# Kernel optimization log

Measured on AMD Instinct MI355X. Metric: run time of the kernel, lower is better.

The kernel has to match this reference:

```python
import jax, jax.numpy as jnp
import numpy as np

B, S, H, NH, L, V, P = 2, 1024, 768, 12, 4, 32000, 1024
HD = H // NH  # head dim = 64; matches scale_val = hidden/num_heads


def setup_inputs() -> dict:
    key = jax.random.key(0)
    ks = jax.random.split(key, 18)
    sc = 0.02
    n = jax.random.normal
    return {
        "input_ids": jax.random.randint(ks[0], (B, S), 0, V, dtype=jnp.int32),
        "seq_mask": jnp.ones((B, S), jnp.float32),
        "bpe_emb": (n(ks[1], (V, H)) * sc).astype(jnp.float32),
        "pos_emb": (n(ks[2], (P, H)) * sc).astype(jnp.float32),
        "qkv_w": (n(ks[3], (L, H, 3 * H)) * sc).astype(jnp.float32),
        "qkv_b": jnp.zeros((L, 3 * H), jnp.float32),
        "res_w": (n(ks[4], (L, H, H)) * sc).astype(jnp.float32),
        "res_b": jnp.zeros((L, H), jnp.float32),
        "ln1_g": jnp.ones((L, H), jnp.float32),
        "ln1_b": jnp.zeros((L, H), jnp.float32),
        "ff1_w": (n(ks[5], (L, H, 4 * H)) * sc).astype(jnp.float32),
        "ff1_b": jnp.zeros((L, 4 * H), jnp.float32),
        "ff2_w": (n(ks[6], (L, 4 * H, H)) * sc).astype(jnp.float32),
        "ff2_b": jnp.zeros((L, H), jnp.float32),
        "ln2_g": jnp.ones((L, H), jnp.float32),
        "ln2_b": jnp.zeros((L, H), jnp.float32),
        "pred_w": (n(ks[7], (H, V)) * sc).astype(jnp.float32),
    }


def _layer_norm(x, g, b, e=1e-5):
    u = jnp.mean(x, -1, keepdims=True)
    s = jnp.mean((x - u) ** 2, -1, keepdims=True)
    return g * ((x - u) / jnp.sqrt(s + e)) + b


def _attention(x, seq_mask, w_qkv, b_qkv, w_res, b_res):
    qkv = x @ w_qkv + b_qkv                    # [B,S,3H]
    q, k, v = jnp.split(qkv, 3, axis=-1)
    q = q.reshape(B, S, NH, HD)
    k = k.reshape(B, S, NH, HD)
    v = v.reshape(B, S, NH, HD)
    score = jnp.einsum('bqhd,bkhd->bhqk', q, k) / jnp.sqrt(jnp.float32(HD))
    tril = jnp.tril(jnp.ones((S, S), jnp.float32))           # causal
    mask = tril[None, None] * seq_mask[:, None, None, :]      # [B,1,S,S]
    score = score + (1.0 - mask) * -1e9
    prob = jax.nn.softmax(score, axis=-1)      # dropout rate 0 -> identity
    val = jnp.einsum('bhqk,bkhd->bqhd', prob, v).reshape(B, S, H)
    return val @ w_res + b_res                 # dropout rate 0 -> identity


def reference(input_ids, seq_mask, bpe_emb, pos_emb, qkv_w, qkv_b, res_w, res_b,
              ln1_g, ln1_b, ff1_w, ff1_b, ff2_w, ff2_b, ln2_g, ln2_b, pred_w):
    pos_idx = jnp.arange(S)
    h = bpe_emb[input_ids] + pos_emb[pos_idx][None]           # [B,S,H]
    for l in range(L):
        a = _attention(h, seq_mask, qkv_w[l], qkv_b[l], res_w[l], res_b[l])
        h = _layer_norm(h + a, ln1_g[l], ln1_b[l])
        m = (jax.nn.gelu(h @ ff1_w[l] + ff1_b[l], approximate=False)
             @ ff2_w[l] + ff2_b[l])
        h = _layer_norm(h + m, ln2_g[l], ln2_b[l])
    pred_score = h @ pred_w                                   # [B,S,V]
    pred_prob = jax.nn.softmax(pred_score, axis=-1)
    return pred_score, pred_prob
```

## Files before the change

kernel.cpp:

```cpp
#include <hip/hip_runtime.h>
#include <math.h>

#define BB 2
#define SS 1024
#define HH 768
#define NHEAD 12
#define HDIM 64
#define NLAYER 4
#define VV 32000
#define MROWS (BB*SS)

typedef unsigned short u16;
typedef __attribute__((ext_vector_type(8))) short short8;
typedef __attribute__((ext_vector_type(4))) float f32x4;
typedef __attribute__((ext_vector_type(4))) unsigned short u16x4;

__device__ __forceinline__ u16 f2bf(float f) {
    union { float f; unsigned u; } x; x.f = f;
    unsigned r = (x.u + 0x7fff + ((x.u >> 16) & 1)) >> 16;
    return (u16)r;
}
__device__ __forceinline__ float bf2f(u16 b) {
    union { unsigned u; float f; } x; x.u = ((unsigned)b) << 16;
    return x.f;
}

__device__ __forceinline__ void gload_lds16(const u16* g, u16* l) {
    __builtin_amdgcn_global_load_lds((const __attribute__((address_space(1))) void*)g,
                                     (__attribute__((address_space(3))) void*)l, 16, 0, 0);
}

__global__ __launch_bounds__(256) void conv_transpose(
    const float* __restrict__ W, u16* __restrict__ Wt, int K, int N) {
    int l = blockIdx.z;
    W  += (size_t)l * K * N;
    Wt += (size_t)l * K * N;
    __shared__ u16 tile[32][33];
    int k0 = blockIdx.y * 32, n0 = blockIdx.x * 32;
    int t = threadIdx.x;
    int ky = t >> 3, nx = (t & 7) * 4;
    float4 v = *(const float4*)(W + (size_t)(k0 + ky) * N + n0 + nx);
    tile[nx + 0][ky] = f2bf(v.x);
    tile[nx + 1][ky] = f2bf(v.y);
    tile[nx + 2][ky] = f2bf(v.z);
    tile[nx + 3][ky] = f2bf(v.w);
    __syncthreads();
    int nr = t >> 3, kc = (t & 7) * 4;
    u16x4 o;
    o[0] = tile[nr][kc + 0]; o[1] = tile[nr][kc + 1];
    o[2] = tile[nr][kc + 2]; o[3] = tile[nr][kc + 3];
    *(u16x4*)(Wt + (size_t)(n0 + nr) * K + k0 + kc) = o;
}

__global__ void embed_kernel(const int* __restrict__ ids,
                             const float* __restrict__ bpe,
                             const float* __restrict__ pos,
                             float* __restrict__ h, u16* __restrict__ hb) {
    int row = blockIdx.x;
    int s = row % SS;
    int id = ids[row];
    const float4* br = (const float4*)(bpe + (size_t)id * HH);
    const float4* pr = (const float4*)(pos + (size_t)s * HH);
    float4* hr = (float4*)(h + (size_t)row * HH);
    u16x4* hbr = (u16x4*)(hb + (size_t)row * HH);
    int t = threadIdx.x;
    float4 a = br[t], c = pr[t];
    a.x += c.x; a.y += c.y; a.z += c.z; a.w += c.w;
    hr[t] = a;
    u16x4 u; u[0] = f2bf(a.x); u[1] = f2bf(a.y); u[2] = f2bf(a.z); u[3] = f2bf(a.w);
    hbr[t] = u;
}

template<int BM, int ACT, int WF32, int WBF>
__global__ __launch_bounds__(256) void mfma_gemm(
    const u16* __restrict__ A, const u16* __restrict__ Wt,
    const float* __restrict__ bias, float* __restrict__ C,
    u16* __restrict__ Cb, int M, int N, int K) {
    constexpr int MR = BM / 32;
    __shared__ u16 As[2 * BM * 32];
    __shared__ u16 Bs[2 * 128 * 32];
    const int tid = threadIdx.x;
    const int lane = tid & 63;
    const int wid = tid >> 6;

    const int nwg = gridDim.x * gridDim.y;
    int id = blockIdx.x + gridDim.x * blockIdx.y;
    int id2 = (nwg & 7) ? id : ((id & 7) * (nwg >> 3) + (id >> 3));
    const int brow = (id2 % gridDim.x) * BM;
    const int bcol = (id2 / gridDim.x) * 128;

    const int wr = (wid >> 1) * (BM / 2);
    const int wc = (wid & 1) * 64;
    f32x4 acc[MR][4] = {};

    const u16* Abase = A + (size_t)brow * K;
    const u16* Bbase = Wt + (size_t)bcol * K;
    const int lrow = lane & 15;
    const int lk = (lane >> 4) * 8;

    auto stage = [&](u16* Ad, u16* Bd, int kt) {
#pragma unroll
        for (int c0 = 0; c0 < BM * 4; c0 += 256) {
            int c = c0 + tid;
            int r = c >> 2, off = (c & 3) * 8;
            gload_lds16(Abase + (size_t)r * K + kt + off, Ad + c * 8);
        }
#pragma unroll
        for (int c0 = 0; c0 < 512; c0 += 256) {
            int c = c0 + tid;
            int r = c >> 2, off = (c & 3) * 8;
            gload_lds16(Bbase + (size_t)r * K + kt + off, Bd + c * 8);
        }
    };

    const int nt = K / 32;
    stage(As, Bs, 0);
    for (int t = 0; t < nt; ++t) {
        u16* Ac = As + (t & 1) * (BM * 32);
        u16* Bc = Bs + (t & 1) * (128 * 32);
        if (t + 1 < nt) {
            stage(As + ((t + 1) & 1) * (BM * 32),
                  Bs + ((t + 1) & 1) * (128 * 32), (t + 1) * 32);
            if constexpr (BM == 128) asm volatile("s_waitcnt vmcnt(4)" ::: "memory");
            else                     asm volatile("s_waitcnt vmcnt(3)" ::: "memory");
        } else {
            asm volatile("s_waitcnt vmcnt(0)" ::: "memory");
        }
        __builtin_amdgcn_s_barrier();
        __builtin_amdgcn_sched_barrier(0);

        short8 a[MR], b[4];
#pragma unroll
        for (int m = 0; m < MR; ++m)
            a[m] = *(const short8*)(Ac + (wr + m * 16 + lrow) * 32 + lk);
#pragma unroll
        for (int n = 0; n < 4; ++n)
            b[n] = *(const short8*)(Bc + (wc + n * 16 + lrow) * 32 + lk);
#pragma unroll
        for (int m = 0; m < MR; ++m)
#pragma unroll
            for (int n = 0; n < 4; ++n)
                acc[m][n] = __builtin_amdgcn_mfma_f32_16x16x32_bf16(a[m], b[n], acc[m][n], 0, 0, 0);

        __builtin_amdgcn_sched_barrier(0);
        __builtin_amdgcn_s_barrier();
    }

    const int lr4 = (lane >> 4) * 4;
#pragma unroll
    for (int n = 0; n < 4; ++n) {
        int col = bcol + wc + n * 16 + lrow;
        float bv = bias ? bias[col] : 0.f;
#pragma unroll
        for (int m = 0; m < MR; ++m) {
#pragma unroll
            for (int j = 0; j < 4; ++j) {
                int row = brow + wr + m * 16 + lr4 + j;
                float v = acc[m][n][j] + bv;
                if (ACT == 1) v = 0.5f * v * (1.f + erff(v * 0.70710678118654752f));
                if (WF32) C[(size_t)row * N + col] = v;
                if (WBF)  Cb[(size_t)row * N + col] = f2bf(v);
            }
        }
    }
}

__global__ __launch_bounds__(256) void attn_kernel(
    const u16* __restrict__ qkvb, const float* __restrict__ seq_mask,
    u16* __restrict__ av) {
    __shared__ u16 Ks[64 * 64];
    __shared__ u16 Vt[64 * 64];
    __shared__ u16 Ps[64 * 64];
    const int qb = gridDim.x - 1 - blockIdx.x;
    const int hd = blockIdx.y, b = blockIdx.z;
    const int t = threadIdx.x;
    const int lane = t & 63;
    const int w = t >> 6;
    const int lrow = lane & 15;
    const int lhi = lane >> 4;
    const int q0 = qb * 64;
    const size_t rs = 3 * HH;

    short8 aq[2];
    {
        const u16* qrow = qkvb + (size_t)(b * SS + q0 + w * 16 + lrow) * rs + hd * HDIM;
        aq[0] = *(const short8*)(qrow + lhi * 8);
        aq[1] = *(const short8*)(qrow + 32 + lhi * 8);
    }

    f32x4 o[4] = {};
    float m_[4] = {-INFINITY, -INFINITY, -INFINITY, -INFINITY};
    float l_[4] = {0.f, 0.f, 0.f, 0.f};

    const int kr = t >> 2, dc = t & 3;
    short8 kA, kB, vA, vB;
    {
        const u16* kbase = qkvb + (size_t)(b * SS + kr) * rs + HH + hd * HDIM + dc * 16;
        kA = *(const short8*)(kbase);
        kB = *(const short8*)(kbase + 8);
        vA = *(const short8*)(kbase + HH);
        vB = *(const short8*)(kbase + HH + 8);
    }

    for (int kt = 0; kt <= qb; ++kt) {
        const int k0 = kt * 64;
        __syncthreads();
        {
            char* krowp = (char*)Ks + kr * 128;
            *(short8*)(krowp + (((dc * 32 + 0)  ^ ((kr & 7) << 4)))) = kA;
            *(short8*)(krowp + (((dc * 32 + 16) ^ ((kr & 7) << 4)))) = kB;
#pragma unroll
            for (int e = 0; e < 8; ++e) {
                int d0 = dc * 16 + e;
                int d1 = dc * 16 + 8 + e;
                *(u16*)((char*)Vt + d0 * 128 + ((kr * 2) ^ ((d0 & 7) << 4))) = (u16)vA[e];
                *(u16*)((char*)Vt + d1 * 128 + ((kr * 2) ^ ((d1 & 7) << 4))) = (u16)vB[e];
            }
        }
        __syncthreads();

        if (kt < qb) {
            const u16* kbase = qkvb + (size_t)(b * SS + k0 + 64 + kr) * rs + HH + hd * HDIM + dc * 16;
            kA = *(const short8*)(kbase);
            kB = *(const short8*)(kbase + 8);
            vA = *(const short8*)(kbase + HH);
            vB = *(const short8*)(kbase + HH + 8);
        }

        f32x4 s[4] = {};
        __builtin_amdgcn_s_setprio(1);
#pragma unroll
        for (int n = 0; n < 4; ++n) {
            const int krow = n * 16 + lrow;
            char* kp = (char*)Ks + krow * 128;
#pragma unroll
            for (int c = 0; c < 2; ++c) {
                short8 bk = *(const short8*)(kp + ((c * 64 + lhi * 16) ^ ((krow & 7) << 4)));
                s[n] = __builtin_amdgcn_mfma_f32_16x16x32_bf16(aq[c], bk, s[n], 0, 0, 0);
            }
        }
        __builtin_amdgcn_s_setprio(0);

        float sm[4];
#pragma unroll
        for (int n = 0; n < 4; ++n) sm[n] = seq_mask[b * SS + k0 + n * 16 + lrow];
        const int diag = (kt == qb);
#pragma unroll
        for (int j = 0; j < 4; ++j) {
            const int qglob = q0 + w * 16 + lhi * 4 + j;
            float sv[4];
#pragma unroll
            for (int n = 0; n < 4; ++n) {
                const int kglob = k0 + n * 16 + lrow;
                float msk = (diag && kglob > qglob) ? 0.f : sm[n];
                sv[n] = s[n][j] * 0.125f + (1.f - msk) * (-1e9f);
            }
            float tm = fmaxf(fmaxf(sv[0], sv[1]), fmaxf(sv[2], sv[3]));
            tm = fmaxf(tm, __shfl_xor(tm, 1));
            tm = fmaxf(tm, __shfl_xor(tm, 2));
            tm = fmaxf(tm, __shfl_xor(tm, 4));
            tm = fmaxf(tm, __shfl_xor(tm, 8));
            float mn = fmaxf(m_[j], tm);
            float sc = __expf(m_[j] - mn);
            float ps = 0.f;
#pragma unroll
            for (int n = 0; n < 4; ++n) {
                float p = __expf(sv[n] - mn);
                s[n][j] = p;
                ps += p;
            }
            ps += __shfl_xor(ps, 1);
            ps += __shfl_xor(ps, 2);
            ps += __shfl_xor(ps, 4);
            ps += __shfl_xor(ps, 8);
            l_[j] = l_[j] * sc + ps;
            m_[j] = mn;
#pragma unroll
            for (int dn = 0; dn < 4; ++dn) o[dn][j] *= sc;
        }

#pragma unroll
        for (int j = 0; j < 4; ++j) {
            const int prow = w * 16 + lhi * 4 + j;
            char* pp = (char*)Ps + prow * 128;
#pragma unroll
            for (int n = 0; n < 4; ++n)
                *(u16*)(pp + ((n * 32 + lrow * 2) ^ ((prow & 7) << 4))) = f2bf(s[n][j]);
        }

        const int arow = w * 16 + lrow;
        char* ap_p = (char*)Ps + arow * 128;
        __builtin_amdgcn_s_setprio(1);
#pragma unroll
        for (int c = 0; c < 2; ++c) {
            short8 ap = *(const short8*)(ap_p + ((c * 64 + lhi * 16) ^ ((arow & 7) << 4)));
#pragma unroll
            for (int dn = 0; dn < 4; ++dn) {
                const int vrow = dn * 16 + lrow;
                short8 bv = *(const short8*)((char*)Vt + vrow * 128 +
                                             ((c * 64 + lhi * 16) ^ ((vrow & 7) << 4)));
                o[dn] = __builtin_amdgcn_mfma_f32_16x16x32_bf16(ap, bv, o[dn], 0, 0, 0);
            }
        }
        __builtin_amdgcn_s_setprio(0);
    }

#pragma unroll
    for (int j = 0; j < 4; ++j) {
        const int q = q0 + w * 16 + lhi * 4 + j;
        const float inv = 1.f / l_[j];
        u16* orow = av + (size_t)(b * SS + q) * HH + hd * HDIM;
#pragma unroll
        for (int dn = 0; dn < 4; ++dn)
            orow[dn * 16 + lrow] = f2bf(o[dn][j] * inv);
    }
}

__global__ void add_ln_kernel(float* __restrict__ h, u16* __restrict__ hb,
                              const float* __restrict__ a,
                              const float* __restrict__ g,
                              const float* __restrict__ bta) {
    int row = blockIdx.x;
    int t = threadIdx.x;
    __shared__ float red[256];
    size_t base = (size_t)row * HH;
    float x0 = h[base + t]       + a[base + t];
    float x1 = h[base + t + 256] + a[base + t + 256];
    float x2 = h[base + t + 512] + a[base + t + 512];

    red[t] = x0 + x1 + x2;
    __syncthreads();
    for (int o = 128; o; o >>= 1) { if (t < o) red[t] += red[t + o]; __syncthreads(); }
    float mean = red[0] * (1.0f / 768.0f);
    __syncthreads();

    float d0 = x0 - mean, d1 = x1 - mean, d2 = x2 - mean;
    red[t] = d0 * d0 + d1 * d1 + d2 * d2;
    __syncthreads();
    for (int o = 128; o; o >>= 1) { if (t < o) red[t] += red[t + o]; __syncthreads(); }
    float var = red[0] * (1.0f / 768.0f);
    float inv = 1.0f / sqrtf(var + 1e-5f);

    float y0 = g[t]       * d0 * inv + bta[t];
    float y1 = g[t + 256] * d1 * inv + bta[t + 256];
    float y2 = g[t + 512] * d2 * inv + bta[t + 512];
    h[base + t] = y0;       hb[base + t] = f2bf(y0);
    h[base + t + 256] = y1; hb[base + t + 256] = f2bf(y1);
    h[base + t + 512] = y2; hb[base + t + 512] = f2bf(y2);
}

__global__ __launch_bounds__(512) void softmax_v_kernel(
    const float* __restrict__ score, float* __restrict__ prob) {
    __shared__ u16 srow[VV];
    __shared__ float red[512];
    int row = blockIdx.x;
    int t = threadIdx.x;
    const float4* sr = (const float4*)(score + (size_t)row * VV);
    float4* pr = (float4*)(prob + (size_t)row * VV);
    const int n4 = VV / 4;

    float mx = -INFINITY;
    for (int i = t; i < n4; i += 512) {
        float4 v = sr[i];
        u16x4 u; u[0] = f2bf(v.x); u[1] = f2bf(v.y); u[2] = f2bf(v.z); u[3] = f2bf(v.w);
        *(u16x4*)(srow + i * 4) = u;
        mx = fmaxf(mx, fmaxf(fmaxf(bf2f(u[0]), bf2f(u[1])), fmaxf(bf2f(u[2]), bf2f(u[3]))));
    }
    red[t] = mx; __syncthreads();
    for (int o = 256; o; o >>= 1) { if (t < o) red[t] = fmaxf(red[t], red[t + o]); __syncthreads(); }
    mx = red[0];
    __syncthreads();

    float s = 0.f;
    for (int i = t; i < n4; i += 512) {
        u16x4 u = *(const u16x4*)(srow + i * 4);
        s += __expf(bf2f(u[0]) - mx) + __expf(bf2f(u[1]) - mx)
           + __expf(bf2f(u[2]) - mx) + __expf(bf2f(u[3]) - mx);
    }
    red[t] = s; __syncthreads();
    for (int o = 256; o; o >>= 1) { if (t < o) red[t] += red[t + o]; __syncthreads(); }
    float inv = 1.0f / red[0];

    for (int i = t; i < n4; i += 512) {
        u16x4 u = *(const u16x4*)(srow + i * 4);
        float4 o4;
        o4.x = __expf(bf2f(u[0]) - mx) * inv; o4.y = __expf(bf2f(u[1]) - mx) * inv;
        o4.z = __expf(bf2f(u[2]) - mx) * inv; o4.w = __expf(bf2f(u[3]) - mx) * inv;
        pr[i] = o4;
    }
}

extern "C" void kernel_launch(void* const* d_in, const int* in_sizes, int n_in,
                              void* d_out, int out_size, void* d_ws, size_t ws_size,
                              hipStream_t stream) {
    const int*   ids      = (const int*)d_in[0];
    const float* seq_mask = (const float*)d_in[1];
    const float* bpe      = (const float*)d_in[2];
    const float* pos      = (const float*)d_in[3];
    const float* qkv_w    = (const float*)d_in[4];
    const float* qkv_b    = (const float*)d_in[5];
    const float* res_w    = (const float*)d_in[6];
    const float* res_b    = (const float*)d_in[7];
    const float* ln1_g    = (const float*)d_in[8];
    const float* ln1_b    = (const float*)d_in[9];
    const float* ff1_w    = (const float*)d_in[10];
    const float* ff1_b    = (const float*)d_in[11];
    const float* ff2_w    = (const float*)d_in[12];
    const float* ff2_b    = (const float*)d_in[13];
    const float* ln2_g    = (const float*)d_in[14];
    const float* ln2_b    = (const float*)d_in[15];
    const float* pred_w   = (const float*)d_in[16];

    float* out_score = (float*)d_out;
    float* out_prob  = out_score + (size_t)MROWS * VV;

    size_t off = 0;
    auto take = [&](size_t bytes) -> size_t {
        size_t p = off; off += (bytes + 255) & ~(size_t)255; return p;
    };
    const size_t o_qkvT = take((size_t)NLAYER * HH * 3 * HH * 2);
    const size_t o_resT = take((size_t)NLAYER * HH * HH * 2);
    const size_t o_ff1T = take((size_t)NLAYER * HH * 4 * HH * 2);
    const size_t o_ff2T = take((size_t)NLAYER * 4 * HH * HH * 2);
    const size_t o_predT = take((size_t)HH * VV * 2);
    const size_t o_h    = take((size_t)MROWS * HH * 4);
    const size_t o_a    = take((size_t)MROWS * HH * 4);
    const size_t o_qkvb = take((size_t)MROWS * 3 * HH * 2);
    const size_t o_hb   = take((size_t)MROWS * HH * 2);
    const size_t o_avb  = take((size_t)MROWS * HH * 2);
    const size_t o_midb = take((size_t)MROWS * 4 * HH * 2);
    const size_t need = off;

    char* arena = (ws_size >= need) ? (char*)d_ws : (char*)out_prob;
    u16*   qkvT = (u16*)(arena + o_qkvT);
    u16*   resT = (u16*)(arena + o_resT);
    u16*   ff1T = (u16*)(arena + o_ff1T);
    u16*   ff2T = (u16*)(arena + o_ff2T);
    u16*   predT = (u16*)(arena + o_predT);
    float* h    = (float*)(arena + o_h);
    float* a    = (float*)(arena + o_a);
    u16*   qkvb = (u16*)(arena + o_qkvb);
    u16*   hb   = (u16*)(arena + o_hb);
    u16*   avb  = (u16*)(arena + o_avb);
    u16*   midb = (u16*)(arena + o_midb);

    conv_transpose<<<dim3(3 * HH / 32, HH / 32, NLAYER), 256, 0, stream>>>(qkv_w, qkvT, HH, 3 * HH);
    conv_transpose<<<dim3(HH / 32, HH / 32, NLAYER), 256, 0, stream>>>(res_w, resT, HH, HH);
    conv_transpose<<<dim3(4 * HH / 32, HH / 32, NLAYER), 256, 0, stream>>>(ff1_w, ff1T, HH, 4 * HH);
    conv_transpose<<<dim3(HH / 32, 4 * HH / 32, NLAYER), 256, 0, stream>>>(ff2_w, ff2T, 4 * HH, HH);
    conv_transpose<<<dim3(VV / 32, HH / 32, 1), 256, 0, stream>>>(pred_w, predT, HH, VV);

    embed_kernel<<<MROWS, 192, 0, stream>>>(ids, bpe, pos, h, hb);

    for (int l = 0; l < NLAYER; ++l) {
        mfma_gemm<128, 0, 0, 1><<<dim3(MROWS / 128, 3 * HH / 128), 256, 0, stream>>>(
            hb, qkvT + (size_t)l * HH * 3 * HH, qkv_b + (size_t)l * 3 * HH,
            nullptr, qkvb, MROWS, 3 * HH, HH);
        attn_kernel<<<dim3(SS / 64, NHEAD, BB), 256, 0, stream>>>(qkvb, seq_mask, avb);
        mfma_gemm<64, 0, 1, 0><<<dim3(MROWS / 64, HH / 128), 256, 0, stream>>>(
            avb, resT + (size_t)l * HH * HH, res_b + (size_t)l * HH,
            a, nullptr, MROWS, HH, HH);
        add_ln_kernel<<<MROWS, 256, 0, stream>>>(h, hb, a,
            ln1_g + (size_t)l * HH, ln1_b + (size_t)l * HH);
        mfma_gemm<128, 1, 0, 1><<<dim3(MROWS / 128, 4 * HH / 128), 256, 0, stream>>>(
            hb, ff1T + (size_t)l * HH * 4 * HH, ff1_b + (size_t)l * 4 * HH,
            nullptr, midb, MROWS, 4 * HH, HH);
        mfma_gemm<64, 0, 1, 0><<<dim3(MROWS / 64, HH / 128), 256, 0, stream>>>(
            midb, ff2T + (size_t)l * 4 * HH * HH, ff2_b + (size_t)l * HH,
            a, nullptr, MROWS, HH, 4 * HH);
        add_ln_kernel<<<MROWS, 256, 0, stream>>>(h, hb, a,
            ln2_g + (size_t)l * HH, ln2_b + (size_t)l * HH);
    }

    mfma_gemm<128, 0, 1, 0><<<dim3(MROWS / 128, VV / 128), 256, 0, stream>>>(
        hb, predT, nullptr, out_score, nullptr, MROWS, VV, HH);
    softmax_v_kernel<<<MROWS, 512, 0, stream>>>(out_score, out_prob);
}
```

Measured before the change: 1.106 ms.

## Double GEMM K-tile to 64 with XOR-swizzled LDS layout

Raises the GEMM K-step from 32 to 64, which halves the number of barrier and wait iterations and doubles the LDS double buffers. An XOR swizzle on the 16-byte chunk index within each 128-byte row is applied in both the global-to-LDS load and the fragment reads, to avoid LDS bank conflicts. The MFMA block is also wrapped in s_setprio raised priority. The cost is higher LDS usage per block, which can reduce occupancy, and the vmcnt wait values are updated to match the doubled load count.

```diff
diff --git a/kernel.cpp b/kernel.cpp
--- a/kernel.cpp
+++ b/kernel.cpp
@@ -77,8 +77,8 @@
     const float* __restrict__ bias, float* __restrict__ C,
     u16* __restrict__ Cb, int M, int N, int K) {
     constexpr int MR = BM / 32;
-    __shared__ u16 As[2 * BM * 32];
-    __shared__ u16 Bs[2 * 128 * 32];
+    __shared__ u16 As[2 * BM * 64];
+    __shared__ u16 Bs[2 * 128 * 64];
     const int tid = threadIdx.x;
     const int lane = tid & 63;
     const int wid = tid >> 6;
@@ -96,51 +96,65 @@
     const u16* Abase = A + (size_t)brow * K;
     const u16* Bbase = Wt + (size_t)bcol * K;
     const int lrow = lane & 15;
-    const int lk = (lane >> 4) * 8;
+    const int lhi = lane >> 4;
 
     auto stage = [&](u16* Ad, u16* Bd, int kt) {
 #pragma unroll
-        for (int c0 = 0; c0 < BM * 4; c0 += 256) {
+        for (int c0 = 0; c0 < BM * 8; c0 += 256) {
             int c = c0 + tid;
-            int r = c >> 2, off = (c & 3) * 8;
-            gload_lds16(Abase + (size_t)r * K + kt + off, Ad + c * 8);
-        }
-#pragma unroll
-        for (int c0 = 0; c0 < 512; c0 += 256) {
+            int r = c >> 3, s = c & 7;
+            gload_lds16(Abase + (size_t)r * K + kt + ((s ^ (r & 7)) * 8), Ad + c * 8);
+        }
+#pragma unroll
+        for (int c0 = 0; c0 < 1024; c0 += 256) {
             int c = c0 + tid;
-            int r = c >> 2, off = (c & 3) * 8;
-            gload_lds16(Bbase + (size_t)r * K + kt + off, Bd + c * 8);
+            int r = c >> 3, s = c & 7;
+            gload_lds16(Bbase + (size_t)r * K + kt + ((s ^ (r & 7)) * 8), Bd + c * 8);
         }
     };
 
-    const int nt = K / 32;
+    const int nt = K / 64;
     stage(As, Bs, 0);
     for (int t = 0; t < nt; ++t) {
-        u16* Ac = As + (t & 1) * (BM * 32);
-        u16* Bc = Bs + (t & 1) * (128 * 32);
+        u16* Ac = As + (t & 1) * (BM * 64);
+        u16* Bc = Bs + (t & 1) * (128 * 64);
         if (t + 1 < nt) {
-            stage(As + ((t + 1) & 1) * (BM * 32),
-                  Bs + ((t + 1) & 1) * (128 * 32), (t + 1) * 32);
-            if constexpr (BM == 128) asm volatile("s_waitcnt vmcnt(4)" ::: "memory");
-            else                     asm volatile("s_waitcnt vmcnt(3)" ::: "memory");
+            stage(As + ((t + 1) & 1) * (BM * 64),
+                  Bs + ((t + 1) & 1) * (128 * 64), (t + 1) * 64);
+            if constexpr (BM == 128) asm volatile("s_waitcnt vmcnt(8)" ::: "memory");
+            else                     asm volatile("s_waitcnt vmcnt(6)" ::: "memory");
         } else {
             asm volatile("s_waitcnt vmcnt(0)" ::: "memory");
         }
         __builtin_amdgcn_s_barrier();
         __builtin_amdgcn_sched_barrier(0);
 
-        short8 a[MR], b[4];
-#pragma unroll
-        for (int m = 0; m < MR; ++m)
-            a[m] = *(const short8*)(Ac + (wr + m * 16 + lrow) * 32 + lk);
-#pragma unroll
-        for (int n = 0; n < 4; ++n)
-            b[n] = *(const short8*)(Bc + (wc + n * 16 + lrow) * 32 + lk);
-#pragma unroll
-        for (int m = 0; m < MR; ++m)
-#pragma unroll
-            for (int n = 0; n < 4; ++n)
-                acc[m][n] = __builtin_amdgcn_mfma_f32_16x16x32_bf16(a[m], b[n], acc[m][n], 0, 0, 0);
+        short8 a[MR][2], b[4][2];
+#pragma unroll
+        for (int m = 0; m < MR; ++m) {
+            const int R = wr + m * 16 + lrow;
+            char* rp = (char*)Ac + R * 128;
+#pragma unroll
+            for (int kk = 0; kk < 2; ++kk)
+                a[m][kk] = *(const short8*)(rp + (((kk * 4 + lhi) ^ (R & 7)) * 16));
+        }
+#pragma unroll
+        for (int n = 0; n < 4; ++n) {
+            const int R = wc + n * 16 + lrow;
+            char* rp = (char*)Bc + R * 128;
+#pragma unroll
+            for (int kk = 0; kk < 2; ++kk)
+                b[n][kk] = *(const short8*)(rp + (((kk * 4 + lhi) ^ (R & 7)) * 16));
+        }
+        __builtin_amdgcn_s_setprio(1);
+#pragma unroll
+        for (int kk = 0; kk < 2; ++kk)
+#pragma unroll
+            for (int m = 0; m < MR; ++m)
+#pragma unroll
+                for (int n = 0; n < 4; ++n)
+                    acc[m][n] = __builtin_amdgcn_mfma_f32_16x16x32_bf16(a[m][kk], b[n][kk], acc[m][n], 0, 0, 0);
+        __builtin_amdgcn_s_setprio(0);
 
         __builtin_amdgcn_sched_barrier(0);
         __builtin_amdgcn_s_barrier();
```

New measurement: 1.032 ms. 6.7% less time.
